# Kernel tuning notes

Measured on AMD Instinct MI355X. Metric: run time of the kernel, lower is better.

## Reference

```python
import jax, jax.numpy as jnp
import numpy as np

GROUP_SIZE = 16777216   # 2**24, output length
PROJ_RATIO = 0.25
INNER = 4194304         # int(GROUP_SIZE * PROJ_RATIO) = 2**22
PADDED = 16777216       # 2**ceil(log2(GROUP_SIZE)) = 2**24
D = 2048                # int(sqrt(INNER))
RANK = 16
ALPHA = 1.0
SCALING = ALPHA / RANK


def setup_inputs() -> dict:
    key = jax.random.key(0)
    kA, kB = jax.random.split(key)
    # LoRA factors (B is zero-init in torch; use small random values so the
    # pipeline produces non-trivial numbers — the math is identical).
    A = jax.random.normal(kA, (RANK, D), dtype=jnp.float32) * 0.02
    Bw = jax.random.normal(kB, (D, RANK), dtype=jnp.float32) * 0.02
    # Fastfood buffers, deterministic as in FastfoodProjection(seed=42)
    rng = np.random.RandomState(42)
    G = jnp.asarray(rng.randn(PADDED), dtype=jnp.float32)
    sign = jnp.asarray(rng.choice([-1, 1], size=PADDED), dtype=jnp.float32)
    perm = jnp.asarray(rng.permutation(PADDED), dtype=jnp.int32)
    return {"A": A, "Bw": Bw, "G": G, "sign": sign, "perm": perm}


def fwht(x):
    """Fast Walsh-Hadamard transform over the last (only) axis, normalized
    by 1/sqrt(n). Same butterfly order as the torch loop: step doubles from 1,
    within each block of 2*step: (a, b) -> (a+b, a-b)."""
    n = x.shape[-1]  # static python int, power of two
    step = 1
    while step < n:
        y = x.reshape(-1, 2, step)               # blocks of 2*step
        x = jnp.concatenate([y[:, :1] + y[:, 1:], y[:, :1] - y[:, 1:]],
                            axis=1).reshape(-1)
        step *= 2
    return x * np.float32(1.0 / np.sqrt(n))


def reference(A, Bw, G, sign, perm):
    # LoRA delta: (D, RANK) @ (RANK, D) * alpha/rank -> (D, D)
    delta = (Bw @ A) * jnp.float32(SCALING)
    flat = delta.reshape(-1)                     # (INNER,)
    flat = jnp.pad(flat, (0, PADDED - INNER))    # zero-pad to 2**24
    # Fastfood: H * G * Pi * H * B
    out = fwht(flat * sign)
    out = out[perm] * G
    out = fwht(out)
    # out_features == GROUP_SIZE == PADDED, so the slice/pad in
    # SuperLoRAGroup.forward is a no-op here; keep it for faithfulness.
    return out[:GROUP_SIZE]
```

## Files before the change

kernel.cpp:

```cpp
#include <hip/hip_runtime.h>


#define THREADS 1024

typedef float vf4 __attribute__((ext_vector_type(4)));
typedef int vi4 __attribute__((ext_vector_type(4)));

constexpr float kScaling = 0.0625f;
constexpr float kNorm = 5.9604644775390625e-8f;

__device__ __forceinline__ void fwht16(float r[16]) {
#pragma unroll
  for (int s = 1; s < 16; s <<= 1) {
#pragma unroll
    for (int i = 0; i < 16; i++) {
      if (!(i & s)) {
        float a = r[i];
        float b = r[i | s];
        r[i] = a + b;
        r[i | s] = a - b;
      }
    }
  }
}

template <bool NT>
__device__ __forceinline__ void fwht_lo_rounds(float* lds, int t, vf4* dst4) {
  vf4* lds4 = (vf4*)lds;
  {
    float r[16];
#pragma unroll
    for (int q = 0; q < 4; q++) {
      vf4 v = lds4[t * 4 + q];
#pragma unroll
      for (int c = 0; c < 4; c++) r[4 * q + c] = v[c];
    }
    fwht16(r);
#pragma unroll
    for (int q = 0; q < 4; q++) {
      vf4 v;
#pragma unroll
      for (int c = 0; c < 4; c++) v[c] = r[4 * q + c];
      lds4[t * 4 + q] = v;
    }
  }
  __syncthreads();
  {
    const int c = (t & 15) | ((t >> 4) << 8);
    float r[16];
#pragma unroll
    for (int k = 0; k < 16; k++) r[k] = lds[c + (k << 4)];
    fwht16(r);
#pragma unroll
    for (int k = 0; k < 16; k++) lds[c + (k << 4)] = r[k];
  }
  __syncthreads();
  {
    const int c = (t & 255) | ((t >> 8) << 12);
    float r[16];
#pragma unroll
    for (int k = 0; k < 16; k++) r[k] = lds[c + (k << 8)];
    fwht16(r);
#pragma unroll
    for (int k = 0; k < 16; k++) lds[c + (k << 8)] = r[k];
  }
  __syncthreads();
  {
    vf4 v0 = lds4[t + 0 * 1024];
    vf4 v1 = lds4[t + 1 * 1024];
    vf4 v2 = lds4[t + 2 * 1024];
    vf4 v3 = lds4[t + 3 * 1024];
    vf4 e0 = v0 + v1, e1 = v0 - v1;
    vf4 e2 = v2 + v3, e3 = v2 - v3;
    vf4 o0 = e0 + e2, o1 = e1 + e3, o2 = e0 - e2, o3 = e1 - e3;
    if (NT) {
      __builtin_nontemporal_store(o0, &dst4[t + 0 * 1024]);
      __builtin_nontemporal_store(o1, &dst4[t + 1 * 1024]);
      __builtin_nontemporal_store(o2, &dst4[t + 2 * 1024]);
      __builtin_nontemporal_store(o3, &dst4[t + 3 * 1024]);
    } else {
      dst4[t + 0 * 1024] = o0;
      dst4[t + 1 * 1024] = o1;
      dst4[t + 2 * 1024] = o2;
      dst4[t + 3 * 1024] = o3;
    }
  }
}

__global__ __launch_bounds__(THREADS) void k1_build_fwht_lo(
    const float* __restrict__ A, const float* __restrict__ Bw,
    const float* __restrict__ sgn, float* __restrict__ W) {
  __shared__ float lds[16384];
  const int t = threadIdx.x;
  const int blk = blockIdx.x;
  const unsigned base = (unsigned)blk << 14;

  float a0[16], a1[16];
#pragma unroll
  for (int k = 0; k < 16; k++) {
    a0[k] = A[k * 2048 + t];
    a1[k] = A[k * 2048 + t + 1024];
  }
  const int r0 = blk * 8;
#pragma unroll
  for (int rl = 0; rl < 8; rl++) {
    float s0 = 0.f, s1 = 0.f;
#pragma unroll
    for (int k = 0; k < 16; k++) {
      float b = Bw[(r0 + rl) * 16 + k];
      s0 += b * a0[k];
      s1 += b * a1[k];
    }
    const int l0 = rl * 2048 + t;
    const int l1 = l0 + 1024;
    lds[l0] = s0 * kScaling * sgn[base + l0];
    lds[l1] = s1 * kScaling * sgn[base + l1];
  }
  __syncthreads();
  fwht_lo_rounds<false>(lds, t, (vf4*)W + ((unsigned)blk << 12));
}

__global__ __launch_bounds__(THREADS) void k_fwht_mid(float* __restrict__ buf) {
  __shared__ float lds[16384];
  vf4* lds4 = (vf4*)lds;
  const int t = threadIdx.x;
  const int seg = blockIdx.x >> 8;
  const int c0 = (blockIdx.x & 255) * 16;
  vf4* B4 = (vf4*)buf + ((unsigned)seg << 20);
#pragma unroll
  for (int m = 0; m < 4; m++) {
    const int idx4 = t + THREADS * m;
    const int row = idx4 >> 4, c4 = idx4 & 15;
    lds4[idx4] = B4[row * 4096 + c0 + c4];
  }
  __syncthreads();
  const int c4 = t & 15;
  const int f = t >> 4;
#pragma unroll
  for (int r = 0; r < 4; r++) {
    const int m = 1 << (2 * r);
    int rows[4];
#pragma unroll
    for (int k2 = 0; k2 < 4; k2++)
      rows[k2] = (f & (m - 1)) + k2 * m + (f >> (2 * r)) * (m << 2);
    vf4 v0 = lds4[rows[0] * 16 + c4];
    vf4 v1 = lds4[rows[1] * 16 + c4];
    vf4 v2 = lds4[rows[2] * 16 + c4];
    vf4 v3 = lds4[rows[3] * 16 + c4];
    vf4 e0 = v0 + v1, e1 = v0 - v1;
    vf4 e2 = v2 + v3, e3 = v2 - v3;
    vf4 o0 = e0 + e2, o1 = e1 + e3, o2 = e0 - e2, o3 = e1 - e3;
    if (r < 3) {
      lds4[rows[0] * 16 + c4] = o0;
      lds4[rows[1] * 16 + c4] = o1;
      lds4[rows[2] * 16 + c4] = o2;
      lds4[rows[3] * 16 + c4] = o3;
      __syncthreads();
    } else {
      B4[rows[0] * 4096 + c0 + c4] = o0;
      B4[rows[1] * 4096 + c0 + c4] = o1;
      B4[rows[2] * 4096 + c0 + c4] = o2;
      B4[rows[3] * 4096 + c0 + c4] = o3;
    }
  }
}

__global__ __launch_bounds__(THREADS) void k3_perm_fwht_lo(
    const float* __restrict__ W, const int* __restrict__ perm,
    const float* __restrict__ G, float* __restrict__ out) {
  __shared__ float lds[16384];
  const int t = threadIdx.x;
  const unsigned base4 = (unsigned)blockIdx.x << 12;
  const vi4* P4 = (const vi4*)perm + base4;
  const vf4* G4 = (const vf4*)G + base4;
  int src[16];
  float gg[16];
#pragma unroll
  for (int m = 0; m < 4; m++) {
    const int idx4 = t + THREADS * m;
    vi4 p = __builtin_nontemporal_load(&P4[idx4]);
    vf4 g = __builtin_nontemporal_load(&G4[idx4]);
#pragma unroll
    for (int c = 0; c < 4; c++) {
      src[4 * m + c] = p[c] & 0x3FFFFF;
      gg[4 * m + c] = g[c] * kNorm;
    }
  }
#pragma unroll
  for (int pass = 0; pass < 4; pass++) {
#pragma unroll
    for (int s = 0; s < 16; s++) {
      if ((src[s] >> 20) == pass) {
        lds[4 * (t + THREADS * (s >> 2)) + (s & 3)] = W[src[s]] * gg[s];
      }
    }
    __syncthreads();
  }
  fwht_lo_rounds<true>(lds, t, (vf4*)out + base4);
}

__global__ __launch_bounds__(THREADS) void k4b_fwht_top(float* __restrict__ out) {
  const unsigned idx4 = blockIdx.x * THREADS + threadIdx.x;
  vf4* O4 = (vf4*)out;
  vf4 v0 = O4[idx4 + 0u * (1u << 20)];
  vf4 v1 = O4[idx4 + 1u * (1u << 20)];
  vf4 v2 = O4[idx4 + 2u * (1u << 20)];
  vf4 v3 = O4[idx4 + 3u * (1u << 20)];
  vf4 e0 = v0 + v1, e1 = v0 - v1;
  vf4 e2 = v2 + v3, e3 = v2 - v3;
  O4[idx4 + 0u * (1u << 20)] = e0 + e2;
  O4[idx4 + 1u * (1u << 20)] = e1 + e3;
  O4[idx4 + 2u * (1u << 20)] = e0 - e2;
  O4[idx4 + 3u * (1u << 20)] = e1 - e3;
}

extern "C" void kernel_launch(void* const* d_in, const int* in_sizes, int n_in,
                              void* d_out, int out_size, void* d_ws,
                              size_t ws_size, hipStream_t stream) {
  (void)in_sizes;
  (void)n_in;
  (void)out_size;
  (void)ws_size;
  const float* A = (const float*)d_in[0];
  const float* Bw = (const float*)d_in[1];
  const float* G = (const float*)d_in[2];
  const float* sgn = (const float*)d_in[3];
  const int* perm = (const int*)d_in[4];
  float* out = (float*)d_out;
  float* W = (float*)d_ws;

  k1_build_fwht_lo<<<256, THREADS, 0, stream>>>(A, Bw, sgn, W);
  k_fwht_mid<<<256, THREADS, 0, stream>>>(W);
  k3_perm_fwht_lo<<<1024, THREADS, 0, stream>>>(W, perm, G, out);
  k_fwht_mid<<<1024, THREADS, 0, stream>>>(out);
  k4b_fwht_top<<<1024, THREADS, 0, stream>>>(out);
}
```

Before: 362.5 us.

## Fuse upper FWHT stages into one LDS kernel and restructure gather waits

Replaces the separate mid-stage FWHT pass and top radix-4 pass on the output with a single kernel that performs all ten upper butterfly levels in LDS, using an XOR swizzle to avoid bank conflicts and a block-index remap. This removes one full read/write sweep of the 64 MB output. The gather kernel now stages G in LDS and issues the permuted W loads across passes with partial vmcnt waits and raw barriers instead of full syncthreads, then multiplies afterwards. The narrow 4-vf4 column strips in the new kernel give strided global accesses, which may reduce coalescing efficiency.

```diff
diff --git a/kernel.cpp b/kernel.cpp
--- a/kernel.cpp
+++ b/kernel.cpp
@@ -165,53 +165,97 @@
   }
 }
 
-__global__ __launch_bounds__(THREADS) void k3_perm_fwht_lo(
+__global__ __launch_bounds__(THREADS, 8) void k3_perm_fwht_lo(
     const float* __restrict__ W, const int* __restrict__ perm,
     const float* __restrict__ G, float* __restrict__ out) {
   __shared__ float lds[16384];
+  vf4* lds4 = (vf4*)lds;
   const int t = threadIdx.x;
   const unsigned base4 = (unsigned)blockIdx.x << 12;
   const vi4* P4 = (const vi4*)perm + base4;
   const vf4* G4 = (const vf4*)G + base4;
   int src[16];
-  float gg[16];
 #pragma unroll
   for (int m = 0; m < 4; m++) {
     const int idx4 = t + THREADS * m;
     vi4 p = __builtin_nontemporal_load(&P4[idx4]);
     vf4 g = __builtin_nontemporal_load(&G4[idx4]);
 #pragma unroll
-    for (int c = 0; c < 4; c++) {
-      src[4 * m + c] = p[c] & 0x3FFFFF;
-      gg[4 * m + c] = g[c] * kNorm;
-    }
-  }
+    for (int c = 0; c < 4; c++) src[4 * m + c] = p[c] & 0x3FFFFF;
+    lds4[idx4] = g * kNorm;
+  }
+  float wv[16];
 #pragma unroll
   for (int pass = 0; pass < 4; pass++) {
 #pragma unroll
     for (int s = 0; s < 16; s++) {
-      if ((src[s] >> 20) == pass) {
-        lds[4 * (t + THREADS * (s >> 2)) + (s & 3)] = W[src[s]] * gg[s];
-      }
-    }
-    __syncthreads();
-  }
+      if ((src[s] >> 20) == pass) wv[s] = W[src[s]];
+    }
+    if (pass < 3) {
+      asm volatile("s_waitcnt vmcnt(8)" ::: "memory");
+      __builtin_amdgcn_s_barrier();
+    }
+  }
+#pragma unroll
+  for (int m = 0; m < 4; m++) {
+    vf4 v = lds4[t + THREADS * m];
+#pragma unroll
+    for (int c = 0; c < 4; c++) v[c] *= wv[4 * m + c];
+    lds4[t + THREADS * m] = v;
+  }
+  __syncthreads();
   fwht_lo_rounds<true>(lds, t, (vf4*)out + base4);
 }
 
-__global__ __launch_bounds__(THREADS) void k4b_fwht_top(float* __restrict__ out) {
-  const unsigned idx4 = blockIdx.x * THREADS + threadIdx.x;
+__global__ __launch_bounds__(THREADS, 8) void k4_fwht_hi(float* __restrict__ out) {
+  __shared__ float lds[16384];
+  vf4* lds4 = (vf4*)lds;
+  const int t = threadIdx.x;
+  const unsigned blk = (blockIdx.x & 7) * 128u + (blockIdx.x >> 3);
+  const unsigned c0 = blk * 4u;
   vf4* O4 = (vf4*)out;
-  vf4 v0 = O4[idx4 + 0u * (1u << 20)];
-  vf4 v1 = O4[idx4 + 1u * (1u << 20)];
-  vf4 v2 = O4[idx4 + 2u * (1u << 20)];
-  vf4 v3 = O4[idx4 + 3u * (1u << 20)];
-  vf4 e0 = v0 + v1, e1 = v0 - v1;
-  vf4 e2 = v2 + v3, e3 = v2 - v3;
-  O4[idx4 + 0u * (1u << 20)] = e0 + e2;
-  O4[idx4 + 1u * (1u << 20)] = e1 + e3;
-  O4[idx4 + 2u * (1u << 20)] = e0 - e2;
-  O4[idx4 + 3u * (1u << 20)] = e1 - e3;
+#pragma unroll
+  for (int m = 0; m < 4; m++) {
+    const int idx4 = t + THREADS * m;
+    const int row = idx4 >> 2, c4 = idx4 & 3;
+    lds4[idx4 ^ ((idx4 >> 4) & 7)] = O4[(unsigned)row * 4096u + c0 + c4];
+  }
+  __syncthreads();
+  const int c4 = t & 3;
+  const int f = t >> 2;
+#pragma unroll
+  for (int r = 0; r < 5; r++) {
+    const int m = 1 << (2 * r);
+    int rows[4];
+#pragma unroll
+    for (int k = 0; k < 4; k++)
+      rows[k] = (f & (m - 1)) + k * m + (f >> (2 * r)) * (m << 2);
+    int sidx[4];
+#pragma unroll
+    for (int k = 0; k < 4; k++) {
+      const int fidx = rows[k] * 4 + c4;
+      sidx[k] = fidx ^ ((fidx >> 4) & 7);
+    }
+    vf4 v0 = lds4[sidx[0]];
+    vf4 v1 = lds4[sidx[1]];
+    vf4 v2 = lds4[sidx[2]];
+    vf4 v3 = lds4[sidx[3]];
+    vf4 e0 = v0 + v1, e1 = v0 - v1;
+    vf4 e2 = v2 + v3, e3 = v2 - v3;
+    vf4 o0 = e0 + e2, o1 = e1 + e3, o2 = e0 - e2, o3 = e1 - e3;
+    if (r < 4) {
+      lds4[sidx[0]] = o0;
+      lds4[sidx[1]] = o1;
+      lds4[sidx[2]] = o2;
+      lds4[sidx[3]] = o3;
+      __syncthreads();
+    } else {
+      __builtin_nontemporal_store(o0, &O4[(unsigned)rows[0] * 4096u + c0 + c4]);
+      __builtin_nontemporal_store(o1, &O4[(unsigned)rows[1] * 4096u + c0 + c4]);
+      __builtin_nontemporal_store(o2, &O4[(unsigned)rows[2] * 4096u + c0 + c4]);
+      __builtin_nontemporal_store(o3, &O4[(unsigned)rows[3] * 4096u + c0 + c4]);
+    }
+  }
 }
 
 extern "C" void kernel_launch(void* const* d_in, const int* in_sizes, int n_in,
@@ -232,6 +276,5 @@
   k1_build_fwht_lo<<<256, THREADS, 0, stream>>>(A, Bw, sgn, W);
   k_fwht_mid<<<256, THREADS, 0, stream>>>(W);
   k3_perm_fwht_lo<<<1024, THREADS, 0, stream>>>(W, perm, G, out);
-  k_fwht_mid<<<1024, THREADS, 0, stream>>>(out);
-  k4b_fwht_top<<<1024, THREADS, 0, stream>>>(out);
-}
+  k4_fwht_hi<<<1024, THREADS, 0, stream>>>(out);
+}
```

New measurement: 354.0 us. 1.02x faster.
